# Kernel tuning notes

Hardware: AMD Instinct MI355X
Metric: run time of the kernel (lower is better)

The kernel has to match this reference:

```python
import jax, jax.numpy as jnp
import numpy as np

N = 50000        # nodes
E = 800000       # edges per meta-path (avg degree 16)
M = 3            # meta-paths
IN = 256         # in_size
HID = 16         # hidden_size (per-head out dim of GATConv)
HEADS = 8
OUT = 8          # out_size (classes)
SA_HID = 128     # StructureAttention hidden_size default
NEG_SLOPE = 0.2  # DGL GATConv leaky_relu default


def setup_inputs() -> dict:
    key = jax.random.key(0)
    ks = jax.random.split(key, 11)
    h = jax.random.normal(ks[0], (N, IN), jnp.float32)
    edges = jax.random.randint(ks[1], (M, 2, E), 0, N, jnp.int32)  # [M, (src,dst), E]
    s = 0.05
    fc_w = jax.random.normal(ks[2], (M, IN, HEADS * HID), jnp.float32) * s
    attn_l = jax.random.normal(ks[3], (M, HEADS, HID), jnp.float32) * s
    attn_r = jax.random.normal(ks[4], (M, HEADS, HID), jnp.float32) * s
    sa_w1 = jax.random.normal(ks[5], (HEADS * HID, SA_HID), jnp.float32) * s
    sa_b1 = jnp.zeros((SA_HID,), jnp.float32)
    sa_w2 = jax.random.normal(ks[6], (SA_HID, 1), jnp.float32) * s
    pred_w = jax.random.normal(ks[7], (HEADS * HID, OUT), jnp.float32) * s
    pred_b = jnp.zeros((OUT,), jnp.float32)
    return {"h": h, "edges": edges, "fc_w": fc_w, "attn_l": attn_l,
            "attn_r": attn_r, "sa_w1": sa_w1, "sa_b1": sa_b1, "sa_w2": sa_w2,
            "pred_w": pred_w, "pred_b": pred_b}


def _gat(h, src, dst, w, al, ar):
    # DGL GATConv, eval mode (dropout=0), activation=elu
    feat = (h @ w).reshape(N, HEADS, HID)                 # [N,H,D]
    el = jnp.einsum('nhd,hd->nh', feat, al)               # [N,H]
    er = jnp.einsum('nhd,hd->nh', feat, ar)               # [N,H]
    e = el[src] + er[dst]                                 # [E,H]
    e = jnp.where(e > 0, e, NEG_SLOPE * e)                # leaky_relu
    # edge softmax over incoming edges of each dst node
    emax = jax.ops.segment_max(e, dst, num_segments=N)    # [N,H]
    ex = jnp.exp(e - emax[dst])                           # [E,H]
    denom = jax.ops.segment_sum(ex, dst, num_segments=N)  # [N,H]
    alpha = ex / denom[dst]                               # [E,H]
    msg = feat[src] * alpha[:, :, None]                   # [E,H,D]
    out = jax.ops.segment_sum(msg, dst, num_segments=N)   # [N,H,D]
    return jax.nn.elu(out).reshape(N, HEADS * HID)        # flatten(1)


def reference(h, edges, fc_w, attn_l, attn_r, sa_w1, sa_b1, sa_w2, pred_w, pred_b):
    # per-meta-path GAT (loop over fixed small set of meta-paths)
    zs = [_gat(h, edges[i, 0], edges[i, 1], fc_w[i], attn_l[i], attn_r[i])
          for i in range(M)]
    z = jnp.stack(zs, axis=1)                             # [N, M, H*D]
    # StructureAttention exactly as in source: softmax over dim 0 (nodes)
    w = jnp.tanh(z @ sa_w1 + sa_b1) @ sa_w2               # [N, M, 1]
    beta = jax.nn.softmax(w, axis=0)                      # softmax over nodes
    fused = (beta * z).sum(0)                             # [M, H*D]
    return fused @ pred_w + pred_b                        # [M, OUT]
```

## Files before the change

### kernel.cpp

```cpp
#include <hip/hip_runtime.h>

#define N_NODES 50000
#define N_EDGES 800000
#define N_META 3
#define IN_DIM 256
#define HD 128
#define HEADS 8
#define HID 16
#define OUT_DIM 8
#define NBKT 196
#define BCAP 5120
#define TILE_E 4096
#define NUMPAD 2064
#define GEMM_BX ((N_NODES + 63) / 64)
#define ELER_BX ((N_NODES * HEADS + 255) / 256)

using bf16x8 = __attribute__((ext_vector_type(8))) short;
using f32x4  = __attribute__((ext_vector_type(4))) float;

__device__ __forceinline__ float bf2f(unsigned short u) {
  union { unsigned int i; float f; } x; x.i = ((unsigned int)u) << 16; return x.f;
}
__device__ __forceinline__ unsigned short f2bf(float f) {
  union { float f; unsigned int i; } x; x.f = f;
  unsigned int r = x.i + 0x7fffu + ((x.i >> 16) & 1u);
  return (unsigned short)(r >> 16);
}
__device__ __forceinline__ float tanh_fast(float x) {
  float e = __expf(2.f * x);
  return 1.f - 2.f / (e + 1.f);
}

__global__ __launch_bounds__(256)
void prep_kernel(const float* __restrict__ fcw, const float* __restrict__ w1,
                 unsigned short* __restrict__ fcwT, unsigned short* __restrict__ w1T) {
  int i = blockIdx.x * 256 + threadIdx.x;
  const int NFC = N_META * IN_DIM * HD;
  if (i < NFC) {
    int p = i / (IN_DIM * HD);
    int rem = i - p * (IN_DIM * HD);
    int k = rem / HD, n = rem - k * HD;
    fcwT[(size_t)p * HD * IN_DIM + n * IN_DIM + k] = f2bf(fcw[i]);
  } else if (i < NFC + HD * HD) {
    int j = i - NFC;
    int k = j / HD, n = j - k * HD;
    w1T[n * HD + k] = f2bf(w1[j]);
  }
}

__global__ __launch_bounds__(256)
void bin_gemm_kernel(const int* __restrict__ edges, int* __restrict__ gcur,
                     unsigned int* __restrict__ bktbuf,
                     const float* __restrict__ A,
                     const unsigned short* __restrict__ BT,
                     unsigned short* __restrict__ Cb, int nrows) {
  __shared__ char smem[15360];
  int p = blockIdx.y;
  int t = threadIdx.x;
  if (blockIdx.x < NBKT) {
    int* hist  = (int*)smem;
    int* gbase = hist + NBKT;
    int* fill  = gbase + NBKT;
    int e0 = blockIdx.x * TILE_E;
    const int* src = edges + (size_t)p * 2 * N_EDGES;
    const int* dst = src + N_EDGES;
    for (int i = t; i < NBKT; i += 256) { hist[i] = 0; fill[i] = 0; }
    __syncthreads();
    for (int i = t; i < TILE_E; i += 256) {
      int e = e0 + i;
      if (e < N_EDGES) atomicAdd(&hist[dst[e] >> 8], 1);
    }
    __syncthreads();
    for (int i = t; i < NBKT; i += 256) {
      int idx = p * NBKT + i;
      gbase[i] = hist[i] ? (idx * BCAP + atomicAdd(&gcur[idx], hist[i])) : 0;
    }
    __syncthreads();
    for (int i = t; i < TILE_E; i += 256) {
      int e = e0 + i;
      if (e < N_EDGES) {
        int d = dst[e];
        int b = d >> 8;
        int r = atomicAdd(&fill[b], 1);
        bktbuf[gbase[b] + r] = ((unsigned int)(d & 255) << 16) | (unsigned int)src[e];
      }
    }
  } else {
    unsigned short* As = (unsigned short*)smem;
    unsigned short* Bs = As + 64 * 40;
    int w = t >> 6, l = t & 63, q = l >> 4, s = l & 15;
    int row0 = (blockIdx.x - NBKT) * 64;
    const unsigned short* BTm = BT + (size_t)p * HD * IN_DIM;
    f32x4 acc[8] = {};
    for (int k0 = 0; k0 < IN_DIM; k0 += 32) {
      {
        int r = t >> 2, c = (t & 3) * 8;
        int gr = row0 + r;
        float4 a0, a1;
        if (gr < nrows) {
          a0 = *(const float4*)(A + (size_t)gr * IN_DIM + k0 + c);
          a1 = *(const float4*)(A + (size_t)gr * IN_DIM + k0 + c + 4);
        } else {
          a0 = make_float4(0.f, 0.f, 0.f, 0.f); a1 = a0;
        }
        ushort4 u0, u1;
        u0.x = f2bf(a0.x); u0.y = f2bf(a0.y); u0.z = f2bf(a0.z); u0.w = f2bf(a0.w);
        u1.x = f2bf(a1.x); u1.y = f2bf(a1.y); u1.z = f2bf(a1.z); u1.w = f2bf(a1.w);
        *(ushort4*)&As[r * 40 + c]     = u0;
        *(ushort4*)&As[r * 40 + c + 4] = u1;
      }
      {
        int n = t >> 1, c = (t & 1) * 16;
        uint4 b0 = *(const uint4*)(BTm + (size_t)n * IN_DIM + k0 + c);
        uint4 b1 = *(const uint4*)(BTm + (size_t)n * IN_DIM + k0 + c + 8);
        *(uint4*)&Bs[n * 40 + c]     = b0;
        *(uint4*)&Bs[n * 40 + c + 8] = b1;
      }
      __syncthreads();
      bf16x8 af = *(bf16x8*)&As[(w * 16 + s) * 40 + q * 8];
      #pragma unroll
      for (int f = 0; f < 8; ++f) {
        bf16x8 bf = *(bf16x8*)&Bs[(f * 16 + s) * 40 + q * 8];
        acc[f] = __builtin_amdgcn_mfma_f32_16x16x32_bf16(af, bf, acc[f], 0, 0, 0);
      }
      __syncthreads();
    }
    unsigned short* Cm = Cb + (size_t)p * N_NODES * HD;
    #pragma unroll
    for (int f = 0; f < 8; ++f) {
      #pragma unroll
      for (int r = 0; r < 4; ++r) {
        int gr = row0 + w * 16 + q * 4 + r;
        if (gr < nrows) Cm[(size_t)gr * HD + f * 16 + s] = f2bf(acc[f][r]);
      }
    }
  }
}

__global__ __launch_bounds__(256)
void sort_eler_kernel(const int* __restrict__ gcur,
                      const unsigned int* __restrict__ bktbuf,
                      int* __restrict__ offsB, int* __restrict__ offsE,
                      int* __restrict__ csr,
                      const unsigned short* __restrict__ featb3,
                      const float* __restrict__ al, const float* __restrict__ ar,
                      float* __restrict__ el3, float* __restrict__ er3) {
  __shared__ int lh[256];
  __shared__ int cur[256];
  __shared__ int wsum[4];
  int p = blockIdx.y;
  int t = threadIdx.x;
  if (blockIdx.x < NBKT) {
    int b = blockIdx.x;
    int lane = t & 63, wid = t >> 6;
    int idx = p * NBKT + b;
    int S = idx * BCAP;
    int E = S + gcur[idx];
    int node0 = b * 256;
    int nn = min(256, N_NODES - node0);
    int gi0 = p * N_NODES + node0;
    lh[t] = 0;
    __syncthreads();
    for (int i = S + t; i < E; i += 256) atomicAdd(&lh[bktbuf[i] >> 16], 1);
    __syncthreads();
    int v = lh[t];
    int s = v;
    #pragma unroll
    for (int d = 1; d < 64; d <<= 1) {
      int x = __shfl_up(s, d);
      if (lane >= d) s += x;
    }
    if (lane == 63) wsum[wid] = s;
    __syncthreads();
    int woff = 0;
    #pragma unroll
    for (int k = 0; k < 4; ++k) if (k < wid) woff += wsum[k];
    int excl = S + woff + s - v;
    if (t < nn) {
      offsB[gi0 + t] = excl;
      offsE[gi0 + t] = excl + v;
    }
    cur[t] = excl;
    __syncthreads();
    for (int i = S + t; i < E; i += 256) {
      unsigned int rec = bktbuf[i];
      int pos = atomicAdd(&cur[rec >> 16], 1);
      csr[pos] = (int)(rec & 0xffffu);
    }
  } else {
    int i = (blockIdx.x - NBKT) * 256 + t;
    if (i >= N_NODES * HEADS) return;
    int node = i >> 3, hh = i & 7;
    const unsigned short* f =
        featb3 + (size_t)p * N_NODES * HD + (size_t)node * HD + hh * HID;
    uint4 u0 = *(const uint4*)(f);
    uint4 u1 = *(const uint4*)(f + 8);
    unsigned int uu[8] = {u0.x, u0.y, u0.z, u0.w, u1.x, u1.y, u1.z, u1.w};
    const float* alm = al + p * HD + hh * HID;
    const float* arm = ar + p * HD + hh * HID;
    float sl = 0.f, sr = 0.f;
    #pragma unroll
    for (int q = 0; q < 8; ++q) {
      float v0 = __uint_as_float(uu[q] << 16);
      float v1 = __uint_as_float(uu[q] & 0xffff0000u);
      int d = q * 2;
      sl += v0 * alm[d] + v1 * alm[d + 1];
      sr += v0 * arm[d] + v1 * arm[d + 1];
    }
    el3[(size_t)p * N_NODES * HEADS + i] = sl;
    er3[(size_t)p * N_NODES * HEADS + i] = sr;
  }
}

__global__ __launch_bounds__(256)
void aggregate_kernel(const int* __restrict__ offsB3, const int* __restrict__ offsE3,
                      const int* __restrict__ csr,
                      const uint4* __restrict__ featb3_u4,
                      const float* __restrict__ el3, const float* __restrict__ er3,
                      uint4* __restrict__ zb3_u4) {
  int m = blockIdx.y;
  int node = blockIdx.x * 4 + (threadIdx.x >> 6);
  if (node >= N_NODES) return;
  const uint4* featb_u4 = featb3_u4 + (size_t)m * N_NODES * 16;
  const float* el = el3 + (size_t)m * N_NODES * HEADS;
  const float* er = er3 + (size_t)m * N_NODES * HEADS;
  uint4* z_u4 = zb3_u4 + (size_t)m * N_NODES * 16;
  int lane = threadIdx.x & 63;
  int qg = lane >> 4;
  int li = lane & 15;
  int ch = li >> 1;
  int beg = offsB3[m * N_NODES + node], end = offsE3[m * N_NODES + node];
  float erh = er[node * HEADS + ch];
  float ssum = 0.f;
  float a[8] = {};
  for (int i = beg; i < end; i += 16) {
    int nk = end - i;
    int last = end - 1;
    int s0 = csr[min(i + qg,      last)];
    int s1 = csr[min(i + qg + 4,  last)];
    int s2 = csr[min(i + qg + 8,  last)];
    int s3 = csr[min(i + qg + 12, last)];
    uint4 v0 = featb_u4[(size_t)s0 * 16 + li];
    uint4 v1 = featb_u4[(size_t)s1 * 16 + li];
    uint4 v2 = featb_u4[(size_t)s2 * 16 + li];
    uint4 v3 = featb_u4[(size_t)s3 * 16 + li];
    float e0 = el[s0 * HEADS + ch] + erh;
    float e1 = el[s1 * HEADS + ch] + erh;
    float e2 = el[s2 * HEADS + ch] + erh;
    float e3 = el[s3 * HEADS + ch] + erh;
    e0 = e0 > 0.f ? e0 : 0.2f * e0;
    e1 = e1 > 0.f ? e1 : 0.2f * e1;
    e2 = e2 > 0.f ? e2 : 0.2f * e2;
    e3 = e3 > 0.f ? e3 : 0.2f * e3;
    float w0 = (qg      < nk) ? __expf(e0) : 0.f;
    float w1 = (qg + 4  < nk) ? __expf(e1) : 0.f;
    float w2 = (qg + 8  < nk) ? __expf(e2) : 0.f;
    float w3 = (qg + 12 < nk) ? __expf(e3) : 0.f;
    ssum += (w0 + w1) + (w2 + w3);
    a[0] += w0 * __uint_as_float(v0.x << 16);
    a[1] += w0 * __uint_as_float(v0.x & 0xffff0000u);
    a[2] += w0 * __uint_as_float(v0.y << 16);
    a[3] += w0 * __uint_as_float(v0.y & 0xffff0000u);
    a[4] += w0 * __uint_as_float(v0.z << 16);
    a[5] += w0 * __uint_as_float(v0.z & 0xffff0000u);
    a[6] += w0 * __uint_as_float(v0.w << 16);
    a[7] += w0 * __uint_as_float(v0.w & 0xffff0000u);
    a[0] += w1 * __uint_as_float(v1.x << 16);
    a[1] += w1 * __uint_as_float(v1.x & 0xffff0000u);
    a[2] += w1 * __uint_as_float(v1.y << 16);
    a[3] += w1 * __uint_as_float(v1.y & 0xffff0000u);
    a[4] += w1 * __uint_as_float(v1.z << 16);
    a[5] += w1 * __uint_as_float(v1.z & 0xffff0000u);
    a[6] += w1 * __uint_as_float(v1.w << 16);
    a[7] += w1 * __uint_as_float(v1.w & 0xffff0000u);
    a[0] += w2 * __uint_as_float(v2.x << 16);
    a[1] += w2 * __uint_as_float(v2.x & 0xffff0000u);
    a[2] += w2 * __uint_as_float(v2.y << 16);
    a[3] += w2 * __uint_as_float(v2.y & 0xffff0000u);
    a[4] += w2 * __uint_as_float(v2.z << 16);
    a[5] += w2 * __uint_as_float(v2.z & 0xffff0000u);
    a[6] += w2 * __uint_as_float(v2.w << 16);
    a[7] += w2 * __uint_as_float(v2.w & 0xffff0000u);
    a[0] += w3 * __uint_as_float(v3.x << 16);
    a[1] += w3 * __uint_as_float(v3.x & 0xffff0000u);
    a[2] += w3 * __uint_as_float(v3.y << 16);
    a[3] += w3 * __uint_as_float(v3.y & 0xffff0000u);
    a[4] += w3 * __uint_as_float(v3.z << 16);
    a[5] += w3 * __uint_as_float(v3.z & 0xffff0000u);
    a[6] += w3 * __uint_as_float(v3.w << 16);
    a[7] += w3 * __uint_as_float(v3.w & 0xffff0000u);
  }
  #pragma unroll
  for (int j = 0; j < 8; ++j) {
    a[j] += __shfl_xor(a[j], 16);
    a[j] += __shfl_xor(a[j], 32);
  }
  ssum += __shfl_xor(ssum, 16);
  ssum += __shfl_xor(ssum, 32);
  float inv = (end > beg) ? 1.f / ssum : 0.f;
  if (qg == 0) {
    #pragma unroll
    for (int j = 0; j < 8; ++j) {
      float z = a[j] * inv;
      a[j] = z > 0.f ? z : __expf(z) - 1.f;
    }
    uint4 o;
    unsigned int p0, p1, p2, p3;
    asm("v_cvt_pk_bf16_f32 %0, %1, %2" : "=v"(p0) : "v"(a[0]), "v"(a[1]));
    asm("v_cvt_pk_bf16_f32 %0, %1, %2" : "=v"(p1) : "v"(a[2]), "v"(a[3]));
    asm("v_cvt_pk_bf16_f32 %0, %1, %2" : "=v"(p2) : "v"(a[4]), "v"(a[5]));
    asm("v_cvt_pk_bf16_f32 %0, %1, %2" : "=v"(p3) : "v"(a[6]), "v"(a[7]));
    o.x = p0; o.y = p1; o.z = p2; o.w = p3;
    z_u4[(size_t)node * 16 + li] = o;
  }
}

__global__ __launch_bounds__(256)
void w_gemm_mfma(const unsigned short* __restrict__ Zb3,
                 const unsigned short* __restrict__ BT,
                 const float* __restrict__ B1, const float* __restrict__ W2,
                 float* __restrict__ numpad3, int nrows) {
  __shared__ unsigned short Bs[128 * 136];
  __shared__ unsigned short As[64 * 136];
  __shared__ float wrow[64];
  __shared__ float part[4][64][2];
  __shared__ float dpart[4];
  int tid = threadIdx.x;
  int m = blockIdx.y;
  const unsigned short* Zb = Zb3 + (size_t)m * N_NODES * HD;
  float* numpad = numpad3 + (size_t)m * NUMPAD;
  int w = tid >> 6, l = tid & 63, q = l >> 4, s = l & 15;
  {
    int n = tid >> 1, c0 = (tid & 1) * 64;
    #pragma unroll
    for (int j = 0; j < 8; ++j)
      *(uint4*)&Bs[n * 136 + c0 + j * 8] = *(const uint4*)(BT + n * HD + c0 + j * 8);
  }
  float b1v[8], w2v[8];
  #pragma unroll
  for (int f = 0; f < 8; ++f) { b1v[f] = B1[f * 16 + s]; w2v[f] = W2[f * 16 + s]; }
  const unsigned int* Zu = (const unsigned int*)Zb;
  float a0 = 0.f, a1 = 0.f, ld = 0.f;
  for (int t = 0; t < 4; ++t) {
    int row0 = blockIdx.x * 256 + t * 64;
    __syncthreads();
    {
      int r = tid >> 2, c0 = (tid & 3) * 32;
      int gr = row0 + r;
      if (gr < nrows) {
        #pragma unroll
        for (int j = 0; j < 4; ++j)
          *(uint4*)&As[r * 136 + c0 + j * 8] =
              *(const uint4*)(Zb + (size_t)gr * HD + c0 + j * 8);
      } else {
        uint4 z = make_uint4(0, 0, 0, 0);
        #pragma unroll
        for (int j = 0; j < 4; ++j) *(uint4*)&As[r * 136 + c0 + j * 8] = z;
      }
    }
    __syncthreads();
    f32x4 acc[8] = {};
    #pragma unroll
    for (int kc = 0; kc < 4; ++kc) {
      bf16x8 af = *(bf16x8*)&As[(w * 16 + s) * 136 + kc * 32 + q * 8];
      #pragma unroll
      for (int f = 0; f < 8; ++f) {
        bf16x8 bf = *(bf16x8*)&Bs[(f * 16 + s) * 136 + kc * 32 + q * 8];
        acc[f] = __builtin_amdgcn_mfma_f32_16x16x32_bf16(af, bf, acc[f], 0, 0, 0);
      }
    }
    #pragma unroll
    for (int r = 0; r < 4; ++r) {
      float p = 0.f;
      #pragma unroll
      for (int f = 0; f < 8; ++f) p += tanh_fast(acc[f][r] + b1v[f]) * w2v[f];
      p += __shfl_xor(p, 1); p += __shfl_xor(p, 2);
      p += __shfl_xor(p, 4); p += __shfl_xor(p, 8);
      if (s == 0) wrow[w * 16 + q * 4 + r] = p;
    }
    __syncthreads();
    for (int r = w; r < 64; r += 4) {
      int gr = row0 + r;
      if (gr < nrows) {
        float e = __expf(wrow[r]);
        unsigned int v = Zu[(size_t)gr * 64 + l];
        a0 += e * __uint_as_float(v << 16);
        a1 += e * __uint_as_float(v & 0xffff0000u);
        if (l == 0) ld += e;
      }
    }
  }
  part[w][l][0] = a0;
  part[w][l][1] = a1;
  if (l == 0) dpart[w] = ld;
  __syncthreads();
  if (w == 0) {
    float s0 = part[0][l][0] + part[1][l][0] + part[2][l][0] + part[3][l][0];
    float s1 = part[0][l][1] + part[1][l][1] + part[2][l][1] + part[3][l][1];
    atomicAdd(&numpad[(2 * l) * 16], s0);
    atomicAdd(&numpad[(2 * l + 1) * 16], s1);
    if (l == 0)
      atomicAdd(&numpad[128 * 16], dpart[0] + dpart[1] + dpart[2] + dpart[3]);
  }
}

__global__ void final_kernel(const float* __restrict__ numpad,
                             const float* __restrict__ PW, const float* __restrict__ PB,
                             float* __restrict__ out) {
  int t = threadIdx.x;
  if (t >= N_META * OUT_DIM) return;
  int m = t >> 3, o = t & 7;
  const float* np = numpad + m * NUMPAD;
  float inv = 1.0f / np[128 * 16];
  float s = 0.f;
  for (int k = 0; k < HD; ++k) s += np[k * 16] * PW[k * OUT_DIM + o];
  out[t] = s * inv + PB[o];
}

extern "C" void kernel_launch(void* const* d_in, const int* in_sizes, int n_in,
                              void* d_out, int out_size, void* d_ws, size_t ws_size,
                              hipStream_t stream) {
  (void)in_sizes; (void)n_in; (void)out_size; (void)ws_size;
  const float* h     = (const float*)d_in[0];
  const int*   edges = (const int*)d_in[1];
  const float* fcw   = (const float*)d_in[2];
  const float* al    = (const float*)d_in[3];
  const float* ar    = (const float*)d_in[4];
  const float* w1    = (const float*)d_in[5];
  const float* b1    = (const float*)d_in[6];
  const float* w2    = (const float*)d_in[7];
  const float* pw    = (const float*)d_in[8];
  const float* pb    = (const float*)d_in[9];
  float* out = (float*)d_out;

  char* ws = (char*)d_ws;
  size_t off = 0;
  auto alloc = [&](size_t bytes) -> void* {
    void* p = ws + off;
    off = (off + bytes + 255) & ~(size_t)255;
    return p;
  };
  unsigned short* featb3 = (unsigned short*)alloc((size_t)N_META * N_NODES * HD * 2);
  unsigned short* zb3    = (unsigned short*)alloc((size_t)N_META * N_NODES * HD * 2);
  unsigned short* fcwT   = (unsigned short*)alloc((size_t)N_META * HD * IN_DIM * 2);
  unsigned short* w1T    = (unsigned short*)alloc((size_t)HD * HD * 2);
  float* el3 = (float*)alloc((size_t)N_META * N_NODES * HEADS * 4);
  float* er3 = (float*)alloc((size_t)N_META * N_NODES * HEADS * 4);
  int* gcur  = (int*)alloc((size_t)N_META * NBKT * 4);
  int* offsB = (int*)alloc((size_t)N_META * N_NODES * 4);
  int* offsE = (int*)alloc((size_t)N_META * N_NODES * 4);
  unsigned int* bktbuf = (unsigned int*)alloc((size_t)N_META * NBKT * BCAP * 4);
  int* csr   = (int*)alloc((size_t)N_META * NBKT * BCAP * 4);
  float* numpad = (float*)alloc((size_t)N_META * NUMPAD * 4);

  hipMemsetAsync(numpad, 0, (size_t)N_META * NUMPAD * 4, stream);
  hipMemsetAsync(gcur, 0, (size_t)N_META * NBKT * 4, stream);

  prep_kernel<<<(N_META * IN_DIM * HD + HD * HD + 255) / 256, 256, 0, stream>>>(
      fcw, w1, fcwT, w1T);

  dim3 agrid_(NBKT + GEMM_BX, N_META);
  bin_gemm_kernel<<<agrid_, 256, 0, stream>>>(
      edges, gcur, bktbuf, h, fcwT, featb3, N_NODES);

  dim3 bgrid_(NBKT + ELER_BX, N_META);
  sort_eler_kernel<<<bgrid_, 256, 0, stream>>>(
      gcur, bktbuf, offsB, offsE, csr, featb3, al, ar, el3, er3);

  dim3 ggrid((N_NODES + 3) / 4, N_META);
  aggregate_kernel<<<ggrid, 256, 0, stream>>>(
      offsB, offsE, csr, (const uint4*)featb3, el3, er3, (uint4*)zb3);

  dim3 wgrid((N_NODES + 255) / 256, N_META);
  w_gemm_mfma<<<wgrid, 256, 0, stream>>>(zb3, w1T, b1, w2, numpad, N_NODES);

  final_kernel<<<1, 64, 0, stream>>>(numpad, pw, pb, out);
}
```

Before: 351.5 us.

## Fuse per-metapath GEMMs to share A tile; fold memsets into prep kernel

The feature GEMM blocks now compute all three meta-path projections at once, so each tile of h is loaded and converted to bf16 once and reused across the three weight matrices. The grid is flattened to one dimension, with the binning blocks indexed by meta-path and bucket. The two hipMemsetAsync calls become extra zeroing work inside prep_kernel to remove launch overhead. The w_gemm kernel reads Z rows from its shared-memory tile instead of reloading them from global memory. The trade-off is more registers (24 accumulators) and larger LDS per block, which may lower occupancy.

```diff
diff --git a/kernel.cpp b/kernel.cpp
--- a/kernel.cpp
+++ b/kernel.cpp
@@ -14,6 +14,7 @@
 #define NUMPAD 2064
 #define GEMM_BX ((N_NODES + 63) / 64)
 #define ELER_BX ((N_NODES * HEADS + 255) / 256)
+#define BING_NB (3 * NBKT)
 
 using bf16x8 = __attribute__((ext_vector_type(8))) short;
 using f32x4  = __attribute__((ext_vector_type(4))) float;
@@ -33,18 +34,26 @@
 
 __global__ __launch_bounds__(256)
 void prep_kernel(const float* __restrict__ fcw, const float* __restrict__ w1,
-                 unsigned short* __restrict__ fcwT, unsigned short* __restrict__ w1T) {
+                 unsigned short* __restrict__ fcwT, unsigned short* __restrict__ w1T,
+                 float* __restrict__ numpad3, int* __restrict__ gcur) {
   int i = blockIdx.x * 256 + threadIdx.x;
   const int NFC = N_META * IN_DIM * HD;
+  const int NW1 = HD * HD;
+  const int NNP = N_META * NUMPAD;
+  const int NGC = N_META * NBKT;
   if (i < NFC) {
     int p = i / (IN_DIM * HD);
     int rem = i - p * (IN_DIM * HD);
     int k = rem / HD, n = rem - k * HD;
     fcwT[(size_t)p * HD * IN_DIM + n * IN_DIM + k] = f2bf(fcw[i]);
-  } else if (i < NFC + HD * HD) {
+  } else if (i < NFC + NW1) {
     int j = i - NFC;
     int k = j / HD, n = j - k * HD;
     w1T[n * HD + k] = f2bf(w1[j]);
+  } else if (i < NFC + NW1 + NNP) {
+    numpad3[i - NFC - NW1] = 0.f;
+  } else if (i < NFC + NW1 + NNP + NGC) {
+    gcur[i - NFC - NW1 - NNP] = 0;
   }
 }
 
@@ -54,14 +63,16 @@
                      const float* __restrict__ A,
                      const unsigned short* __restrict__ BT,
                      unsigned short* __restrict__ Cb, int nrows) {
-  __shared__ char smem[15360];
-  int p = blockIdx.y;
+  __shared__ char smem[35840];
   int t = threadIdx.x;
-  if (blockIdx.x < NBKT) {
+  int bx = blockIdx.x;
+  if (bx < BING_NB) {
+    int p = bx / NBKT;
+    int b = bx - p * NBKT;
     int* hist  = (int*)smem;
     int* gbase = hist + NBKT;
     int* fill  = gbase + NBKT;
-    int e0 = blockIdx.x * TILE_E;
+    int e0 = b * TILE_E;
     const int* src = edges + (size_t)p * 2 * N_EDGES;
     const int* dst = src + N_EDGES;
     for (int i = t; i < NBKT; i += 256) { hist[i] = 0; fill[i] = 0; }
@@ -80,18 +91,17 @@
       int e = e0 + i;
       if (e < N_EDGES) {
         int d = dst[e];
-        int b = d >> 8;
-        int r = atomicAdd(&fill[b], 1);
-        bktbuf[gbase[b] + r] = ((unsigned int)(d & 255) << 16) | (unsigned int)src[e];
+        int b2 = d >> 8;
+        int r = atomicAdd(&fill[b2], 1);
+        bktbuf[gbase[b2] + r] = ((unsigned int)(d & 255) << 16) | (unsigned int)src[e];
       }
     }
   } else {
     unsigned short* As = (unsigned short*)smem;
     unsigned short* Bs = As + 64 * 40;
     int w = t >> 6, l = t & 63, q = l >> 4, s = l & 15;
-    int row0 = (blockIdx.x - NBKT) * 64;
-    const unsigned short* BTm = BT + (size_t)p * HD * IN_DIM;
-    f32x4 acc[8] = {};
+    int row0 = (bx - BING_NB) * 64;
+    f32x4 acc[3][8] = {};
     for (int k0 = 0; k0 < IN_DIM; k0 += 32) {
       {
         int r = t >> 2, c = (t & 3) * 8;
@@ -111,27 +121,39 @@
       }
       {
         int n = t >> 1, c = (t & 1) * 16;
-        uint4 b0 = *(const uint4*)(BTm + (size_t)n * IN_DIM + k0 + c);
-        uint4 b1 = *(const uint4*)(BTm + (size_t)n * IN_DIM + k0 + c + 8);
-        *(uint4*)&Bs[n * 40 + c]     = b0;
-        *(uint4*)&Bs[n * 40 + c + 8] = b1;
+        #pragma unroll
+        for (int mm = 0; mm < 3; ++mm) {
+          const unsigned short* BTm =
+              BT + (size_t)mm * HD * IN_DIM + (size_t)n * IN_DIM + k0 + c;
+          uint4 b0 = *(const uint4*)(BTm);
+          uint4 b1 = *(const uint4*)(BTm + 8);
+          unsigned short* Bsm = Bs + mm * (128 * 40) + n * 40 + c;
+          *(uint4*)&Bsm[0] = b0;
+          *(uint4*)&Bsm[8] = b1;
+        }
       }
       __syncthreads();
       bf16x8 af = *(bf16x8*)&As[(w * 16 + s) * 40 + q * 8];
       #pragma unroll
+      for (int mm = 0; mm < 3; ++mm) {
+        #pragma unroll
+        for (int f = 0; f < 8; ++f) {
+          bf16x8 bfv = *(bf16x8*)&Bs[mm * (128 * 40) + (f * 16 + s) * 40 + q * 8];
+          acc[mm][f] = __builtin_amdgcn_mfma_f32_16x16x32_bf16(af, bfv, acc[mm][f], 0, 0, 0);
+        }
+      }
+      __syncthreads();
+    }
+    #pragma unroll
+    for (int mm = 0; mm < 3; ++mm) {
+      unsigned short* Cm = Cb + (size_t)mm * N_NODES * HD;
+      #pragma unroll
       for (int f = 0; f < 8; ++f) {
-        bf16x8 bf = *(bf16x8*)&Bs[(f * 16 + s) * 40 + q * 8];
-        acc[f] = __builtin_amdgcn_mfma_f32_16x16x32_bf16(af, bf, acc[f], 0, 0, 0);
-      }
-      __syncthreads();
-    }
-    unsigned short* Cm = Cb + (size_t)p * N_NODES * HD;
-    #pragma unroll
-    for (int f = 0; f < 8; ++f) {
-      #pragma unroll
-      for (int r = 0; r < 4; ++r) {
-        int gr = row0 + w * 16 + q * 4 + r;
-        if (gr < nrows) Cm[(size_t)gr * HD + f * 16 + s] = f2bf(acc[f][r]);
+        #pragma unroll
+        for (int r = 0; r < 4; ++r) {
+          int gr = row0 + w * 16 + q * 4 + r;
+          if (gr < nrows) Cm[(size_t)gr * HD + f * 16 + s] = f2bf(acc[mm][f][r]);
+        }
       }
     }
   }
@@ -339,7 +361,6 @@
   float b1v[8], w2v[8];
   #pragma unroll
   for (int f = 0; f < 8; ++f) { b1v[f] = B1[f * 16 + s]; w2v[f] = W2[f * 16 + s]; }
-  const unsigned int* Zu = (const unsigned int*)Zb;
   float a0 = 0.f, a1 = 0.f, ld = 0.f;
   for (int t = 0; t < 4; ++t) {
     int row0 = blockIdx.x * 256 + t * 64;
@@ -383,7 +404,7 @@
       int gr = row0 + r;
       if (gr < nrows) {
         float e = __expf(wrow[r]);
-        unsigned int v = Zu[(size_t)gr * 64 + l];
+        unsigned int v = *(const unsigned int*)&As[r * 136 + 2 * l];
         a0 += e * __uint_as_float(v << 16);
         a1 += e * __uint_as_float(v & 0xffff0000u);
         if (l == 0) ld += e;
@@ -453,14 +474,11 @@
   int* csr   = (int*)alloc((size_t)N_META * NBKT * BCAP * 4);
   float* numpad = (float*)alloc((size_t)N_META * NUMPAD * 4);
 
-  hipMemsetAsync(numpad, 0, (size_t)N_META * NUMPAD * 4, stream);
-  hipMemsetAsync(gcur, 0, (size_t)N_META * NBKT * 4, stream);
-
-  prep_kernel<<<(N_META * IN_DIM * HD + HD * HD + 255) / 256, 256, 0, stream>>>(
-      fcw, w1, fcwT, w1T);
-
-  dim3 agrid_(NBKT + GEMM_BX, N_META);
-  bin_gemm_kernel<<<agrid_, 256, 0, stream>>>(
+  const int PREP_N = N_META * IN_DIM * HD + HD * HD + N_META * NUMPAD + N_META * NBKT;
+  prep_kernel<<<(PREP_N + 255) / 256, 256, 0, stream>>>(
+      fcw, w1, fcwT, w1T, numpad, gcur);
+
+  bin_gemm_kernel<<<BING_NB + GEMM_BX, 256, 0, stream>>>(
       edges, gcur, bktbuf, h, fcwT, featb3, N_NODES);
 
   dim3 bgrid_(NBKT + ELER_BX, N_META);
```

After: 344.3 us. 2.0% less time.
